# Performance work log

Measured on AMD Instinct MI355X. Metric: run time of the kernel, lower is better.

The kernel has to match this reference:

```python
import jax, jax.numpy as jnp
import numpy as np

D_MODEL = 2816
D_DENSE = 2112
N_EXPERTS = 128
G = 16
P = 8
D_FFN = 704
EPS = 1e-6
TOP_K = 8
H = 16
DH = 256
NKV = 8
MAX_CTX = 4096
WINDOW = 1024


def rmsnorm(x, w=None):
    h = x.astype(jnp.float32)
    h = h * jax.lax.rsqrt(jnp.mean(h * h, axis=-1, keepdims=True) + EPS)
    if w is not None:
        h = h * (1.0 + w.astype(jnp.float32))
    return h.astype(x.dtype)


def apply_rope(x, cos, sin):
    # x: (1,T,heads,D); cos/sin: (1,T,D)
    cos = cos[:, :, None, :]
    sin = sin[:, :, None, :]
    d = x.shape[-1]
    x1, x2 = x[..., : d // 2], x[..., d // 2 :]
    rot = jnp.concatenate([-x2, x1], axis=-1)
    return x * cos + rot * sin


def setup_inputs() -> dict:
    key = jax.random.key(0)
    ks = iter(jax.random.split(key, 40))
    def rn(shape, s=0.02):
        return jax.random.normal(next(ks), shape, jnp.float32) * s
    pos = MAX_CTX - 1
    half = DH // 2
    inv = 1.0 / (10000.0 ** (np.arange(half, dtype=np.float32) / half))
    ang = pos * inv
    cos = jnp.asarray(np.concatenate([np.cos(ang), np.cos(ang)]).astype(np.float32))[None, None, :]
    sin = jnp.asarray(np.concatenate([np.sin(ang), np.sin(ang)]).astype(np.float32))[None, None, :]
    idx = np.arange(MAX_CTX)
    allowed = (idx <= pos) & (idx > pos - WINDOW)
    attn_mask = jnp.asarray(np.where(allowed, 0.0, -1e9).astype(np.float32))[None, None, None, :]
    wm = np.zeros((1, 1, MAX_CTX, 1), np.float32)
    wm[0, 0, pos, 0] = 1.0
    return {
        "x": rn((1, 1, D_MODEL), 1.0),
        "cos": cos,
        "sin": sin,
        "k_cache": rn((1, NKV, MAX_CTX, DH), 0.02),
        "v_cache": rn((1, NKV, MAX_CTX, DH), 0.02),
        "attn_mask": attn_mask,
        "kv_write_mask": jnp.asarray(wm),
        "input_ln_w": rn((D_MODEL,), 0.1),
        "post_attn_ln_w": rn((D_MODEL,), 0.1),
        "pre_ffn_ln_w": rn((D_MODEL,), 0.1),
        "post_ffn_ln_1_w": rn((D_MODEL,), 0.1),
        "pre_ffn_ln_2_w": rn((D_MODEL,), 0.1),
        "post_ffn_ln_2_w": rn((D_MODEL,), 0.1),
        "post_ffn_ln_w": rn((D_MODEL,), 0.1),
        "Wq": rn((H * DH, D_MODEL)),
        "Wk": rn((NKV * DH, D_MODEL)),
        "Wv": rn((NKV * DH, D_MODEL)),
        "Wo": rn((D_MODEL, H * DH)),
        "q_norm_w": rn((DH,), 0.1),
        "k_norm_w": rn((DH,), 0.1),
        "dense_Wg": rn((D_DENSE, D_MODEL)),
        "dense_Wu": rn((D_DENSE, D_MODEL)),
        "dense_Wd": rn((D_MODEL, D_DENSE)),
        "router_Wp": rn((N_EXPERTS, D_MODEL)),
        "router_scale": jnp.ones((D_MODEL,), jnp.float32),
        "router_pes": jnp.ones((N_EXPERTS,), jnp.float32),
        "packs_Wg": rn((P, G * D_FFN, D_MODEL)),
        "packs_Wu": rn((P, G * D_FFN, D_MODEL)),
        "packs_Wd": rn((P, G * D_MODEL, D_FFN)),
        "layer_scalar": jnp.ones((1,), jnp.float32),
    }


def reference(x, cos, sin, k_cache, v_cache, attn_mask, kv_write_mask,
              input_ln_w, post_attn_ln_w, pre_ffn_ln_w, post_ffn_ln_1_w,
              pre_ffn_ln_2_w, post_ffn_ln_2_w, post_ffn_ln_w,
              Wq, Wk, Wv, Wo, q_norm_w, k_norm_w,
              dense_Wg, dense_Wu, dense_Wd,
              router_Wp, router_scale, router_pes,
              packs_Wg, packs_Wu, packs_Wd, layer_scalar):
    # ---- attention block ----
    residual = x
    h = rmsnorm(x, input_ln_w)
    q = (h @ Wq.T).reshape(1, 1, H, DH)
    k = (h @ Wk.T).reshape(1, 1, NKV, DH)
    v = (h @ Wv.T).reshape(1, 1, NKV, DH)
    q = apply_rope(rmsnorm(q, q_norm_w), cos, sin)
    k = apply_rope(rmsnorm(k, k_norm_w), cos, sin)
    v = rmsnorm(v)
    q = q.transpose(0, 2, 1, 3)            # (1,H,1,DH)
    k = k.transpose(0, 2, 1, 3)            # (1,NKV,1,DH)
    v = v.transpose(0, 2, 1, 3)
    k_new = k_cache + k * kv_write_mask    # one-hot write at current pos
    v_new = v_cache + v * kv_write_mask
    rep = H // NKV
    K = jnp.repeat(k_new, rep, axis=1)     # (1,H,CTX,DH)
    V = jnp.repeat(v_new, rep, axis=1)
    scores = jnp.einsum('bhqd,bhkd->bhqk', q, K) + attn_mask
    w = jax.nn.softmax(scores.astype(jnp.float32), axis=-1).astype(q.dtype)
    ctx = jnp.einsum('bhqk,bhkd->bhqd', w, V)
    ctx = ctx.transpose(0, 2, 1, 3).reshape(1, 1, H * DH)
    a = ctx @ Wo.T
    x1 = residual + rmsnorm(a, post_attn_ln_w)
    # ---- FFN block ----
    res2 = x1
    pre = rmsnorm(x1, pre_ffn_ln_w)
    dense = (jax.nn.gelu(pre @ dense_Wg.T, approximate=True) * (pre @ dense_Wu.T)) @ dense_Wd.T
    h1 = rmsnorm(dense, post_ffn_ln_1_w)
    # router (top-k over 128 experts, scatter to dense weights)
    hr = rmsnorm(res2) * router_scale * (D_MODEL ** -0.5)
    prob = jax.nn.softmax(jnp.einsum('btd,ed->bte', hr, router_Wp), axis=-1)
    topw, topi = jax.lax.top_k(prob, TOP_K)
    topw = topw / jnp.sum(topw, axis=-1, keepdims=True)
    topw = topw * router_pes[topi]
    onehot = (topi[..., None] == jnp.arange(N_EXPERTS)).astype(topw.dtype)
    rw = jnp.sum(topw[..., None] * onehot, axis=-2)          # (1,1,128)
    # packed experts: block-diagonal form of the GxG batched GEMM + diagonal gather
    pre2 = rmsnorm(res2, pre_ffn_ln_2_w)
    xv = pre2.reshape(D_MODEL)
    g = jax.nn.gelu(jnp.einsum('d,pfd->pf', xv, packs_Wg), approximate=True)
    u = jnp.einsum('d,pfd->pf', xv, packs_Wu)
    hh = (g * u).reshape(P, G, D_FFN)
    Wd3 = packs_Wd.reshape(P, G, D_MODEL, D_FFN)
    per_e = jnp.einsum('pgf,pgdf->pgd', hh, Wd3)             # per-expert outputs
    moe = jnp.einsum('pg,pgd->d', rw.reshape(P, G), per_e).reshape(1, 1, D_MODEL)
    h2 = rmsnorm(moe, post_ffn_ln_2_w)
    x_ffn = rmsnorm(h1 + h2, post_ffn_ln_w)
    out = (res2 + x_ffn) * layer_scalar
    return (out, k_new, v_new)
```

## Files before the change

### kernel.cpp

```cpp
#include <hip/hip_runtime.h>
#include <hip/hip_bf16.h>
#include <math.h>

#define D_MODEL 2816
#define DM4 704
#define D_DENSE 2112
#define N_EXPERTS 128
#define D_FFN 704
#define DF4 176
#define TOPK 8
#define H 16
#define DH 256
#define NKV 8
#define MAX_CTX 4096
#define EPS 1e-6f

__device__ __forceinline__ float wsum(float v){
  #pragma unroll
  for(int o=32;o>0;o>>=1) v += __shfl_down(v, o, 64);
  return v;
}
__device__ __forceinline__ float wmax(float v){
  #pragma unroll
  for(int o=32;o>0;o>>=1) v = fmaxf(v, __shfl_down(v, o, 64));
  return v;
}
__device__ __forceinline__ float wsum_all(float v){
  #pragma unroll
  for(int o=32;o>0;o>>=1) v += __shfl_xor(v, o, 64);
  return v;
}
__device__ __forceinline__ float wmax_all(float v){
  #pragma unroll
  for(int o=32;o>0;o>>=1) v = fmaxf(v, __shfl_xor(v, o, 64));
  return v;
}
__device__ __forceinline__ int wmin_all_i(int v){
  #pragma unroll
  for(int o=32;o>0;o>>=1) v = min(v, __shfl_xor(v, o, 64));
  return v;
}
__device__ __forceinline__ float block_sum(float v, float* sm){
  int lane = threadIdx.x & 63, w = threadIdx.x >> 6;
  int nw = blockDim.x >> 6;
  v = wsum(v);
  __syncthreads();
  if (lane == 0) sm[w] = v;
  __syncthreads();
  float t = 0.f;
  for (int i = 0; i < nw; i++) t += sm[i];
  return t;
}
__device__ __forceinline__ float gelu_tanh(float x){
  float x3 = x*x*x;
  return 0.5f*x*(1.f + tanhf(0.7978845608028654f*(x + 0.044715f*x3)));
}
__device__ __forceinline__ float dot4(float4 a, float4 b){
  return fmaf(a.x,b.x, fmaf(a.y,b.y, fmaf(a.z,b.z, a.w*b.w)));
}

__global__ __launch_bounds__(256) void k_qkv(const float* __restrict__ Wq,
    const float* __restrict__ Wk, const float* __restrict__ Wv,
    const float* __restrict__ x, const float* __restrict__ lw,
    float* __restrict__ out){
  __shared__ float sh[D_MODEL];
  __shared__ float sm[8];
  int t = threadIdx.x;
  float xv[11]; float ss = 0.f;
  #pragma unroll
  for (int i=0;i<11;i++){ xv[i] = x[t + 256*i]; ss += xv[i]*xv[i]; }
  ss = block_sum(ss, sm);
  float r = rsqrtf(ss/(float)D_MODEL + EPS);
  #pragma unroll
  for (int i=0;i<11;i++){ int idx=t+256*i; sh[idx] = xv[i]*r*(1.f+lw[idx]); }
  __syncthreads();

  int row = blockIdx.x*4 + (t>>6);
  int lane = t & 63;
  const float* W; int rr;
  if (row < 4096){ W=Wq; rr=row; }
  else if (row < 6144){ W=Wk; rr=row-4096; }
  else { W=Wv; rr=row-6144; }
  const float4* wr = (const float4*)(W + (size_t)rr*D_MODEL);
  const float4* hv = (const float4*)sh;
  float acc=0.f;
  for (int i=lane;i<DM4;i+=64) acc += dot4(wr[i], hv[i]);
  acc = wsum(acc);
  if (lane==0) out[row]=acc;
}

__global__ __launch_bounds__(256) void k_headnorm(const float* __restrict__ qkv,
    const float* __restrict__ qw, const float* __restrict__ kw,
    const float* __restrict__ cs, const float* __restrict__ sn,
    float* __restrict__ qf, float* __restrict__ kf, float* __restrict__ vf){
  __shared__ float sm[8];
  __shared__ float nb[DH];
  int b = blockIdx.x, t = threadIdx.x;
  const float* src; float* dst; const float* w = nullptr; bool rope=false;
  if (b < 16){ src=qkv + b*DH; dst=qf + b*DH; w=qw; rope=true; }
  else if (b < 24){ int hh=b-16; src=qkv+4096+hh*DH; dst=kf+hh*DH; w=kw; rope=true; }
  else { int hh=b-24; src=qkv+6144+hh*DH; dst=vf+hh*DH; }
  float v = src[t];
  float ss = block_sum(v*v, sm);
  float r = rsqrtf(ss/(float)DH + EPS);
  float nv = v*r*(w ? (1.f+w[t]) : 1.f);
  nb[t]=nv;
  __syncthreads();
  float o = nv;
  if (rope){
    float rot = (t < 128) ? -nb[t+128] : nb[t-128];
    o = nv*cs[t] + rot*sn[t];
  }
  dst[t]=o;
}

__global__ __launch_bounds__(256) void k_kvattn(const float* __restrict__ kc,
    const float* __restrict__ vc, const float* __restrict__ kf,
    const float* __restrict__ vf, const float* __restrict__ qf,
    const float* __restrict__ wm, const float* __restrict__ mask,
    float* __restrict__ ko, float* __restrict__ vo, float* __restrict__ part){
  int bid = blockIdx.x;
  if (bid < 4096){
    const size_t TOT = (size_t)NKV*MAX_CTX*(DH/4);
    const size_t stride = (size_t)4096*256;
    for (size_t i = (size_t)bid*256 + threadIdx.x; i < 2*TOT; i += stride){
      int isv = i >= TOT;
      size_t j = isv ? i - TOT : i;
      int pos  = (int)((j >> 6) & (MAX_CTX-1));
      int head = (int)(j >> 18);
      int d4   = (int)(j & 63);
      float m = wm[pos];
      float4 c = ((const float4*)(isv ? vc : kc))[j];
      float4 a = ((const float4*)((isv ? vf : kf) + head*DH))[d4];
      c.x = fmaf(a.x, m, c.x); c.y = fmaf(a.y, m, c.y);
      c.z = fmaf(a.z, m, c.z); c.w = fmaf(a.w, m, c.w);
      ((float4*)(isv ? vo : ko))[j] = c;
    }
    return;
  }
  __shared__ float sc[256];
  __shared__ float sw[256];
  __shared__ float sm[8];
  int abid = bid - 4096;
  int head = abid >> 4, chunk = abid & 15;
  int kvh = head >> 1;
  int lane = threadIdx.x & 63, wv = threadIdx.x >> 6;
  int t = threadIdx.x;
  int base = chunk*256;
  float mk_t = mask[base + t];
  float live = block_sum((mk_t > -1e8f) ? 1.f : 0.f, sm);
  float* p = part + (size_t)(head*16+chunk)*258;
  if (live == 0.f){
    if (t == 0){ p[0] = -3.0e38f; p[1] = 0.f; }
    return;
  }
  float4 q  = ((const float4*)(qf + head*DH))[lane];
  float4 kp = ((const float4*)(kf + kvh*DH))[lane];
  float vp  = vf[kvh*DH + t];
  const float* K = kc + (size_t)kvh*MAX_CTX*DH;
  const float* V = vc + (size_t)kvh*MAX_CTX*DH;
  for (int i=0;i<64;i++){
    int pp = wv*64 + i;
    int pos = base + pp;
    float mk = mask[pos];
    float s = -3.0e38f;
    if (mk > -1e8f){
      float m = wm[pos];
      float4 kv = ((const float4*)(K + (size_t)pos*DH))[lane];
      kv.x = fmaf(kp.x, m, kv.x); kv.y = fmaf(kp.y, m, kv.y);
      kv.z = fmaf(kp.z, m, kv.z); kv.w = fmaf(kp.w, m, kv.w);
      float d = wsum(dot4(q, kv));
      s = d + mk;
    }
    if (lane==0) sc[pp] = s;
  }
  __syncthreads();
  float sv = sc[t];
  float mx = wmax(sv);
  __syncthreads();
  if (lane==0) sm[wv]=mx;
  __syncthreads();
  mx = fmaxf(fmaxf(sm[0],sm[1]),fmaxf(sm[2],sm[3]));
  float w = (sv > -1e30f) ? __expf(sv - mx) : 0.f;
  sw[t] = w;
  float ssum = block_sum(w, sm);
  float acc = 0.f;
  for (int i=0;i<256;i++){
    float wi = sw[i];
    if (wi != 0.f){
      float v = fmaf(vp, wm[base+i], V[(size_t)(base+i)*DH + t]);
      acc = fmaf(wi, v, acc);
    }
  }
  if (t==0){ p[0]=mx; p[1]=ssum; }
  p[2+t]=acc;
}

__global__ __launch_bounds__(256) void k_attn_comb(const float* __restrict__ part,
    float* __restrict__ ctx){
  int head = blockIdx.x, t = threadIdx.x;
  float M = -3.0e38f;
  for (int c=0;c<16;c++) M = fmaxf(M, part[(size_t)(head*16+c)*258]);
  float tot = 0.f, acc = 0.f;
  for (int c=0;c<16;c++){
    const float* p = part + (size_t)(head*16+c)*258;
    float mc=p[0], scv=p[1];
    if (scv > 0.f){
      float f = __expf(mc - M);
      tot = fmaf(scv, f, tot);
      acc = fmaf(f, p[2+t], acc);
    }
  }
  ctx[head*DH + t] = acc / tot;
}

__global__ __launch_bounds__(256) void k_gemv(const float* __restrict__ W,
    const float* __restrict__ x, float* __restrict__ y, int rows, int k4){
  int row = blockIdx.x*4 + (threadIdx.x>>6);
  int lane = threadIdx.x & 63;
  if (row >= rows) return;
  const float4* wr = (const float4*)W + (size_t)row*k4;
  const float4* xv = (const float4*)x;
  float acc = 0.f;
  for (int i=lane;i<k4;i+=64) acc += dot4(wr[i], xv[i]);
  acc = wsum(acc);
  if (lane==0) y[row]=acc;
}

__global__ __launch_bounds__(256) void k_postattn(const float* __restrict__ a,
    const float* __restrict__ x, const float* __restrict__ wpost,
    const float* __restrict__ wpre, const float* __restrict__ rscale,
    const float* __restrict__ wpre2,
    float* __restrict__ x1, float* __restrict__ pre,
    float* __restrict__ hr, float* __restrict__ pre2){
  __shared__ float sm[8];
  int t = threadIdx.x;
  float av[11]; float ss=0.f;
  #pragma unroll
  for (int i=0;i<11;i++){ av[i]=a[t+256*i]; ss += av[i]*av[i]; }
  ss = block_sum(ss, sm);
  float ra = rsqrtf(ss/(float)D_MODEL + EPS);
  float xv[11]; float ss2=0.f;
  #pragma unroll
  for (int i=0;i<11;i++){
    int idx=t+256*i;
    xv[i] = x[idx] + av[i]*ra*(1.f+wpost[idx]);
    ss2 += xv[i]*xv[i];
  }
  ss2 = block_sum(ss2, sm);
  float r1 = rsqrtf(ss2/(float)D_MODEL + EPS);
  const float invsq = rsqrtf((float)D_MODEL);
  #pragma unroll
  for (int i=0;i<11;i++){
    int idx=t+256*i;
    float n = xv[i]*r1;
    x1[idx]=xv[i];
    pre[idx]=n*(1.f+wpre[idx]);
    hr[idx]=n*rscale[idx]*invsq;
    pre2[idx]=n*(1.f+wpre2[idx]);
  }
}

__global__ __launch_bounds__(256) void k_dense_gu_router(const float* __restrict__ Wg,
    const float* __restrict__ Wu, const float* __restrict__ pre,
    const float* __restrict__ Wp, const float* __restrict__ hr,
    float* __restrict__ act, float* __restrict__ lg){
  int lane = threadIdx.x & 63;
  int wv = threadIdx.x >> 6;
  if (blockIdx.x < 528){
    int row = blockIdx.x*4 + wv;
    const float4* g4 = (const float4*)(Wg + (size_t)row*D_MODEL);
    const float4* u4 = (const float4*)(Wu + (size_t)row*D_MODEL);
    const float4* xv = (const float4*)pre;
    float ag=0.f, au=0.f;
    for (int i=lane;i<DM4;i+=64){
      float4 b = xv[i];
      ag += dot4(g4[i], b);
      au += dot4(u4[i], b);
    }
    ag = wsum(ag); au = wsum(au);
    if (lane==0) act[row] = gelu_tanh(ag)*au;
  } else {
    int row = (blockIdx.x-528)*4 + wv;
    const float4* wr = (const float4*)(Wp + (size_t)row*D_MODEL);
    const float4* xv = (const float4*)hr;
    float acc = 0.f;
    for (int i=lane;i<DM4;i+=64) acc += dot4(wr[i], xv[i]);
    acc = wsum(acc);
    if (lane==0) lg[row]=acc;
  }
}

__global__ __launch_bounds__(64) void k_topk(const float* __restrict__ lg,
    const float* __restrict__ pes, float* __restrict__ selw, int* __restrict__ seli){
  int lane = threadIdx.x;
  float l0 = lg[lane], l1 = lg[lane+64];
  float m = wmax_all(fmaxf(l0,l1));
  float e0 = __expf(l0-m), e1 = __expf(l1-m);
  float s = wsum_all(e0+e1);
  float p0 = e0/s, p1 = e1/s;
  float vals[8]; int idxs[8]; float tw=0.f;
  #pragma unroll
  for (int ts=0;ts<8;ts++){
    float mx = wmax_all(fmaxf(p0,p1));
    int cand = 0x7fffffff;
    if (p0 == mx) cand = lane;
    else if (p1 == mx) cand = lane + 64;
    int imin = wmin_all_i(cand);
    if (imin == lane) p0 = -1.f;
    else if (imin == lane+64) p1 = -1.f;
    vals[ts]=mx; idxs[ts]=imin; tw += mx;
  }
  if (lane == 0){
    #pragma unroll
    for (int ts=0;ts<8;ts++){
      selw[ts] = vals[ts]/tw*pes[idxs[ts]];
      seli[ts] = idxs[ts];
    }
  }
}

__global__ __launch_bounds__(256) void k_ddown_moegu(const float* __restrict__ Wd,
    const float* __restrict__ act, float* __restrict__ dense,
    const float* __restrict__ pWg, const float* __restrict__ pWu,
    const float* __restrict__ pre2, const int* __restrict__ seli,
    float* __restrict__ hh){
  int lane = threadIdx.x & 63;
  int wv = threadIdx.x >> 6;
  if (blockIdx.x < 704){
    int row = blockIdx.x*4 + wv;
    const float4* wr = (const float4*)(Wd + (size_t)row*D_DENSE);
    const float4* xv = (const float4*)act;
    float acc = 0.f;
    for (int i=lane;i<528;i+=64) acc += dot4(wr[i], xv[i]);
    acc = wsum(acc);
    if (lane==0) dense[row]=acc;
  } else {
    int gidx = (blockIdx.x-704)*4 + wv;
    int sl = gidx / D_FFN;
    int f = gidx - sl*D_FFN;
    int e = seli[sl];
    int p = e >> 4, g = e & 15;
    size_t ro = ((size_t)p*(16*D_FFN) + (size_t)g*D_FFN + f)*D_MODEL;
    const float4* g4 = (const float4*)(pWg + ro);
    const float4* u4 = (const float4*)(pWu + ro);
    const float4* xv = (const float4*)pre2;
    float ag=0.f, au=0.f;
    for (int i=lane;i<DM4;i+=64){
      float4 b=xv[i];
      ag += dot4(g4[i], b);
      au += dot4(u4[i], b);
    }
    ag = wsum(ag); au = wsum(au);
    if (lane==0) hh[sl*D_FFN + f] = gelu_tanh(ag)*au;
  }
}

__global__ __launch_bounds__(256) void k_moe_down(const float* __restrict__ Wd,
    const float* __restrict__ hh, const int* __restrict__ seli,
    float* __restrict__ pere){
  int gidx = blockIdx.x*4 + (threadIdx.x>>6);
  int lane = threadIdx.x & 63;
  int sl = gidx / D_MODEL;
  int d = gidx - sl*D_MODEL;
  int e = seli[sl];
  int p = e >> 4, g = e & 15;
  const float4* wr = (const float4*)(Wd + ((size_t)p*(16*D_MODEL) + (size_t)g*D_MODEL + d)*D_FFN);
  const float4* xv = (const float4*)(hh + sl*D_FFN);
  float acc=0.f;
  for (int i=lane;i<DF4;i+=64) acc += dot4(wr[i], xv[i]);
  acc = wsum(acc);
  if (lane==0) pere[sl*D_MODEL + d] = acc;
}

__global__ __launch_bounds__(256) void k_final(const float* __restrict__ pere,
    const float* __restrict__ selw, const float* __restrict__ dense,
    const float* __restrict__ x1, const float* __restrict__ w2,
    const float* __restrict__ w1, const float* __restrict__ wf,
    const float* __restrict__ lsc, float* __restrict__ out){
  __shared__ float sm[8];
  int t = threadIdx.x;
  float mo[11], dn[11]; float ssm_=0.f, ssd=0.f;
  #pragma unroll
  for (int i=0;i<11;i++){
    int idx=t+256*i;
    float mv=0.f;
    #pragma unroll
    for (int s=0;s<TOPK;s++) mv = fmaf(selw[s], pere[s*D_MODEL+idx], mv);
    mo[i]=mv; ssm_ += mv*mv;
    dn[i]=dense[idx]; ssd += dn[i]*dn[i];
  }
  ssm_ = block_sum(ssm_, sm);
  ssd = block_sum(ssd, sm);
  float rm = rsqrtf(ssm_/(float)D_MODEL + EPS);
  float rd = rsqrtf(ssd/(float)D_MODEL + EPS);
  float tv[11]; float sst=0.f;
  #pragma unroll
  for (int i=0;i<11;i++){
    int idx=t+256*i;
    float h2 = mo[i]*rm*(1.f+w2[idx]);
    float h1 = dn[i]*rd*(1.f+w1[idx]);
    tv[i]=h1+h2; sst += tv[i]*tv[i];
  }
  sst = block_sum(sst, sm);
  float rt = rsqrtf(sst/(float)D_MODEL + EPS);
  float l = lsc[0];
  #pragma unroll
  for (int i=0;i<11;i++){
    int idx=t+256*i;
    out[idx] = (x1[idx] + tv[i]*rt*(1.f+wf[idx]))*l;
  }
}

extern "C" void kernel_launch(void* const* d_in, const int* in_sizes, int n_in,
                              void* d_out, int out_size, void* d_ws, size_t ws_size,
                              hipStream_t stream){
  const float* x        = (const float*)d_in[0];
  const float* cs       = (const float*)d_in[1];
  const float* sn       = (const float*)d_in[2];
  const float* kc       = (const float*)d_in[3];
  const float* vc       = (const float*)d_in[4];
  const float* mask     = (const float*)d_in[5];
  const float* wm       = (const float*)d_in[6];
  const float* in_ln    = (const float*)d_in[7];
  const float* post_attn= (const float*)d_in[8];
  const float* pre_ffn  = (const float*)d_in[9];
  const float* post_ffn1= (const float*)d_in[10];
  const float* pre_ffn2 = (const float*)d_in[11];
  const float* post_ffn2= (const float*)d_in[12];
  const float* post_ffn = (const float*)d_in[13];
  const float* Wq       = (const float*)d_in[14];
  const float* Wk       = (const float*)d_in[15];
  const float* Wv       = (const float*)d_in[16];
  const float* Wo       = (const float*)d_in[17];
  const float* qnw      = (const float*)d_in[18];
  const float* knw      = (const float*)d_in[19];
  const float* dWg      = (const float*)d_in[20];
  const float* dWu      = (const float*)d_in[21];
  const float* dWd      = (const float*)d_in[22];
  const float* rWp      = (const float*)d_in[23];
  const float* rscale   = (const float*)d_in[24];
  const float* rpes     = (const float*)d_in[25];
  const float* pWg      = (const float*)d_in[26];
  const float* pWu      = (const float*)d_in[27];
  const float* pWd      = (const float*)d_in[28];
  const float* lsc      = (const float*)d_in[29];

  float* out = (float*)d_out;
  float* ko  = out + D_MODEL;
  float* vo  = ko + (size_t)NKV*MAX_CTX*DH;

  float* ws   = (float*)d_ws;
  float* qkv  = ws + 0;
  float* qf   = ws + 8192;
  float* kf   = ws + 12288;
  float* vf   = ws + 14336;
  float* ctx  = ws + 16384;
  float* a    = ws + 20480;
  float* x1   = ws + 23296;
  float* pre  = ws + 26112;
  float* hr   = ws + 28928;
  float* pre2 = ws + 31744;
  float* act  = ws + 34560;
  float* dense= ws + 36672;
  float* lg   = ws + 39488;
  float* selw = ws + 39616;
  int*   seli = (int*)(ws + 39624);
  float* hh   = ws + 39632;
  float* pere = ws + 45264;
  float* part = ws + 67792;

  k_qkv            <<<2048, 256, 0, stream>>>(Wq, Wk, Wv, x, in_ln, qkv);
  k_headnorm       <<<32,   256, 0, stream>>>(qkv, qnw, knw, cs, sn, qf, kf, vf);
  k_kvattn         <<<4352, 256, 0, stream>>>(kc, vc, kf, vf, qf, wm, mask, ko, vo, part);
  k_attn_comb      <<<16,   256, 0, stream>>>(part, ctx);
  k_gemv           <<<704,  256, 0, stream>>>(Wo, ctx, a, D_MODEL, 1024);
  k_postattn       <<<1,    256, 0, stream>>>(a, x, post_attn, pre_ffn, rscale, pre_ffn2,
                                              x1, pre, hr, pre2);
  k_dense_gu_router<<<560,  256, 0, stream>>>(dWg, dWu, pre, rWp, hr, act, lg);
  k_topk           <<<1,     64, 0, stream>>>(lg, rpes, selw, seli);
  k_ddown_moegu    <<<2112, 256, 0, stream>>>(dWd, act, dense, pWg, pWu, pre2, seli, hh);
  k_moe_down       <<<5632, 256, 0, stream>>>(pWd, hh, seli, pere);
  k_final          <<<1,    256, 0, stream>>>(pere, selw, dense, x1,
                                              post_ffn2, post_ffn1, post_ffn, lsc, out);
}
```

Measured before the change: 254.3 us.

## Fuse small kernels via last-block atomic counters, cutting launches from eleven to six

Merges headnorm into the attention/KV-copy kernel, with each block recomputing its own q/k/v normalization and RoPE. The attention combine, post-attention norm, top-k and final norm are moved into the tail of the preceding kernels using a threadfence plus atomic counter, so the last block to finish does the reduction. Counters are zeroed in the first kernel. This removes several tiny single-block launches and their gaps, at the cost of redundant head-norm work per block and a serialized tail block in each fused kernel.

New measurement: 781.9 us. +207.5%, slower.

```diff
diff --git a/kernel.cpp b/kernel.cpp
--- a/kernel.cpp
+++ b/kernel.cpp
@@ -62,10 +62,11 @@
 __global__ __launch_bounds__(256) void k_qkv(const float* __restrict__ Wq,
     const float* __restrict__ Wk, const float* __restrict__ Wv,
     const float* __restrict__ x, const float* __restrict__ lw,
-    float* __restrict__ out){
+    float* __restrict__ out, int* __restrict__ cnt){
   __shared__ float sh[D_MODEL];
   __shared__ float sm[8];
   int t = threadIdx.x;
+  if (blockIdx.x == 0 && t < 32) cnt[t] = 0;
   float xv[11]; float ss = 0.f;
   #pragma unroll
   for (int i=0;i<11;i++){ xv[i] = x[t + 256*i]; ss += xv[i]*xv[i]; }
@@ -89,184 +90,223 @@
   if (lane==0) out[row]=acc;
 }
 
-__global__ __launch_bounds__(256) void k_headnorm(const float* __restrict__ qkv,
+__global__ __launch_bounds__(256) void k_attn_copy(
+    const float* __restrict__ kc, const float* __restrict__ vc,
+    const float* __restrict__ qkv,
     const float* __restrict__ qw, const float* __restrict__ kw,
     const float* __restrict__ cs, const float* __restrict__ sn,
-    float* __restrict__ qf, float* __restrict__ kf, float* __restrict__ vf){
+    const float* __restrict__ wm, const float* __restrict__ mask,
+    float* __restrict__ ko, float* __restrict__ vo,
+    float* __restrict__ part, float* __restrict__ ctx, int* __restrict__ cnt){
   __shared__ float sm[8];
-  __shared__ float nb[DH];
-  int b = blockIdx.x, t = threadIdx.x;
-  const float* src; float* dst; const float* w = nullptr; bool rope=false;
-  if (b < 16){ src=qkv + b*DH; dst=qf + b*DH; w=qw; rope=true; }
-  else if (b < 24){ int hh=b-16; src=qkv+4096+hh*DH; dst=kf+hh*DH; w=kw; rope=true; }
-  else { int hh=b-24; src=qkv+6144+hh*DH; dst=vf+hh*DH; }
-  float v = src[t];
-  float ss = block_sum(v*v, sm);
-  float r = rsqrtf(ss/(float)DH + EPS);
-  float nv = v*r*(w ? (1.f+w[t]) : 1.f);
-  nb[t]=nv;
-  __syncthreads();
-  float o = nv;
-  if (rope){
-    float rot = (t < 128) ? -nb[t+128] : nb[t-128];
-    o = nv*cs[t] + rot*sn[t];
-  }
-  dst[t]=o;
-}
-
-__global__ __launch_bounds__(256) void k_kvattn(const float* __restrict__ kc,
-    const float* __restrict__ vc, const float* __restrict__ kf,
-    const float* __restrict__ vf, const float* __restrict__ qf,
-    const float* __restrict__ wm, const float* __restrict__ mask,
-    float* __restrict__ ko, float* __restrict__ vo, float* __restrict__ part){
-  int bid = blockIdx.x;
-  if (bid < 4096){
-    const size_t TOT = (size_t)NKV*MAX_CTX*(DH/4);
-    const size_t stride = (size_t)4096*256;
-    for (size_t i = (size_t)bid*256 + threadIdx.x; i < 2*TOT; i += stride){
-      int isv = i >= TOT;
-      size_t j = isv ? i - TOT : i;
-      int pos  = (int)((j >> 6) & (MAX_CTX-1));
-      int head = (int)(j >> 18);
-      int d4   = (int)(j & 63);
+  int t = threadIdx.x;
+
+  if (blockIdx.x >= 256){
+    __shared__ float nrm[DH];
+    int b = blockIdx.x - 256;
+    int tensor = b >> 11;
+    int head = (b >> 8) & 7;
+    int blk = b & 255;
+    const float* src = qkv + (tensor ? 6144 : 4096) + head*DH;
+    float v = src[t];
+    float ssq = block_sum(v*v, sm);
+    float r = rsqrtf(ssq/(float)DH + EPS);
+    float base_ = v*r*(tensor==0 ? (1.f+kw[t]) : 1.f);
+    nrm[t] = base_;
+    __syncthreads();
+    float nv = base_;
+    if (tensor == 0){
+      float rot = (t<128) ? -nrm[t+128] : nrm[t-128];
+      nv = base_*cs[t] + rot*sn[t];
+    }
+    __syncthreads();
+    nrm[t] = nv;
+    __syncthreads();
+    const float4* cache = (const float4*)(tensor ? vc : kc);
+    float4* outp = (float4*)(tensor ? vo : ko);
+    const float4* a4 = (const float4*)nrm;
+    size_t hb = (size_t)head * (MAX_CTX*(DH/4));
+    int lbase = blk*1024;
+    #pragma unroll
+    for (int q=0;q<4;q++){
+      int jl = lbase + q*256 + t;
+      int pos = jl >> 6;
+      int d4 = jl & 63;
       float m = wm[pos];
-      float4 c = ((const float4*)(isv ? vc : kc))[j];
-      float4 a = ((const float4*)((isv ? vf : kf) + head*DH))[d4];
-      c.x = fmaf(a.x, m, c.x); c.y = fmaf(a.y, m, c.y);
-      c.z = fmaf(a.z, m, c.z); c.w = fmaf(a.w, m, c.w);
-      ((float4*)(isv ? vo : ko))[j] = c;
+      float4 c = cache[hb + jl];
+      float4 a = a4[d4];
+      c.x = fmaf(a.x,m,c.x); c.y = fmaf(a.y,m,c.y);
+      c.z = fmaf(a.z,m,c.z); c.w = fmaf(a.w,m,c.w);
+      outp[hb + jl] = c;
     }
     return;
   }
-  __shared__ float sc[256];
-  __shared__ float sw[256];
-  __shared__ float sm[8];
-  int abid = bid - 4096;
-  int head = abid >> 4, chunk = abid & 15;
+
+  __shared__ float qrow[DH], krow[DH], vrow[DH], sc[256], sw[256];
+  int head = blockIdx.x >> 4, chunk = blockIdx.x & 15;
   int kvh = head >> 1;
-  int lane = threadIdx.x & 63, wv = threadIdx.x >> 6;
-  int t = threadIdx.x;
+  int lane = t & 63, wv = t >> 6;
+
+  {
+    float v = qkv[head*DH + t];
+    float ssq = block_sum(v*v, sm);
+    float r = rsqrtf(ssq/(float)DH + EPS);
+    float b_ = v*r*(1.f+qw[t]);
+    qrow[t]=b_;
+    __syncthreads();
+    float rot = (t<128) ? -qrow[t+128] : qrow[t-128];
+    float nv = b_*cs[t] + rot*sn[t];
+    __syncthreads();
+    qrow[t]=nv;
+  }
+  {
+    float v = qkv[4096 + kvh*DH + t];
+    float ssq = block_sum(v*v, sm);
+    float r = rsqrtf(ssq/(float)DH + EPS);
+    float b_ = v*r*(1.f+kw[t]);
+    krow[t]=b_;
+    __syncthreads();
+    float rot = (t<128) ? -krow[t+128] : krow[t-128];
+    float nv = b_*cs[t] + rot*sn[t];
+    __syncthreads();
+    krow[t]=nv;
+  }
+  {
+    float v = qkv[6144 + kvh*DH + t];
+    float ssq = block_sum(v*v, sm);
+    vrow[t] = v*rsqrtf(ssq/(float)DH + EPS);
+  }
+  __syncthreads();
+
   int base = chunk*256;
   float mk_t = mask[base + t];
   float live = block_sum((mk_t > -1e8f) ? 1.f : 0.f, sm);
   float* p = part + (size_t)(head*16+chunk)*258;
-  if (live == 0.f){
+  if (live != 0.f){
+    float4 q  = ((const float4*)qrow)[lane];
+    float4 kp = ((const float4*)krow)[lane];
+    float vp  = vrow[t];
+    const float* K = kc + (size_t)kvh*MAX_CTX*DH;
+    const float* V = vc + (size_t)kvh*MAX_CTX*DH;
+    for (int i=0;i<64;i++){
+      int pp = wv*64 + i;
+      int pos = base + pp;
+      float mk = mask[pos];
+      float s = -3.0e38f;
+      if (mk > -1e8f){
+        float m = wm[pos];
+        float4 kv = ((const float4*)(K + (size_t)pos*DH))[lane];
+        kv.x = fmaf(kp.x, m, kv.x); kv.y = fmaf(kp.y, m, kv.y);
+        kv.z = fmaf(kp.z, m, kv.z); kv.w = fmaf(kp.w, m, kv.w);
+        float d = wsum(dot4(q, kv));
+        s = d + mk;
+      }
+      if (lane==0) sc[pp] = s;
+    }
+    __syncthreads();
+    float sv = sc[t];
+    float mx = wmax(sv);
+    __syncthreads();
+    if (lane==0) sm[wv]=mx;
+    __syncthreads();
+    mx = fmaxf(fmaxf(sm[0],sm[1]),fmaxf(sm[2],sm[3]));
+    float w = (sv > -1e30f) ? __expf(sv - mx) : 0.f;
+    sw[t] = w;
+    float ssum = block_sum(w, sm);
+    float acc = 0.f;
+    for (int i=0;i<256;i++){
+      float wi = sw[i];
+      if (wi != 0.f){
+        float v = fmaf(vp, wm[base+i], V[(size_t)(base+i)*DH + t]);
+        acc = fmaf(wi, v, acc);
+      }
+    }
+    if (t==0){ p[0]=mx; p[1]=ssum; }
+    p[2+t]=acc;
+  } else {
     if (t == 0){ p[0] = -3.0e38f; p[1] = 0.f; }
-    return;
-  }
-  float4 q  = ((const float4*)(qf + head*DH))[lane];
-  float4 kp = ((const float4*)(kf + kvh*DH))[lane];
-  float vp  = vf[kvh*DH + t];
-  const float* K = kc + (size_t)kvh*MAX_CTX*DH;
-  const float* V = vc + (size_t)kvh*MAX_CTX*DH;
-  for (int i=0;i<64;i++){
-    int pp = wv*64 + i;
-    int pos = base + pp;
-    float mk = mask[pos];
-    float s = -3.0e38f;
-    if (mk > -1e8f){
-      float m = wm[pos];
-      float4 kv = ((const float4*)(K + (size_t)pos*DH))[lane];
-      kv.x = fmaf(kp.x, m, kv.x); kv.y = fmaf(kp.y, m, kv.y);
-      kv.z = fmaf(kp.z, m, kv.z); kv.w = fmaf(kp.w, m, kv.w);
-      float d = wsum(dot4(q, kv));
-      s = d + mk;
-    }
-    if (lane==0) sc[pp] = s;
-  }
-  __syncthreads();
-  float sv = sc[t];
-  float mx = wmax(sv);
-  __syncthreads();
-  if (lane==0) sm[wv]=mx;
-  __syncthreads();
-  mx = fmaxf(fmaxf(sm[0],sm[1]),fmaxf(sm[2],sm[3]));
-  float w = (sv > -1e30f) ? __expf(sv - mx) : 0.f;
-  sw[t] = w;
-  float ssum = block_sum(w, sm);
+  }
+
+  __threadfence();
+  __syncthreads();
+  __shared__ int lastf;
+  if (t==0) lastf = (atomicAdd(&cnt[head],1) == 15);
+  __syncthreads();
+  if (lastf){
+    __threadfence();
+    float M = -3.0e38f;
+    for (int c=0;c<16;c++) M = fmaxf(M, part[(size_t)(head*16+c)*258]);
+    float tot = 0.f, acc = 0.f;
+    for (int c=0;c<16;c++){
+      const float* pc = part + (size_t)(head*16+c)*258;
+      float mc=pc[0], scv=pc[1];
+      if (scv > 0.f){
+        float f = __expf(mc - M);
+        tot = fmaf(scv, f, tot);
+        acc = fmaf(f, pc[2+t], acc);
+      }
+    }
+    ctx[head*DH + t] = acc / tot;
+  }
+}
+
+__global__ __launch_bounds__(256) void k_wo_post(const float* __restrict__ Wo,
+    const float* __restrict__ ctxv, const float* __restrict__ x,
+    const float* __restrict__ wpost, const float* __restrict__ wpre,
+    const float* __restrict__ rscale, const float* __restrict__ wpre2,
+    float* __restrict__ a, float* __restrict__ x1, float* __restrict__ pre,
+    float* __restrict__ hr, float* __restrict__ pre2, int* __restrict__ cnt){
+  __shared__ float sm[8];
+  int t = threadIdx.x, lane = t & 63, wv = t >> 6;
+  int row = blockIdx.x*4 + wv;
+  const float4* wr = (const float4*)(Wo + (size_t)row*4096);
+  const float4* xv = (const float4*)ctxv;
   float acc = 0.f;
-  for (int i=0;i<256;i++){
-    float wi = sw[i];
-    if (wi != 0.f){
-      float v = fmaf(vp, wm[base+i], V[(size_t)(base+i)*DH + t]);
-      acc = fmaf(wi, v, acc);
-    }
-  }
-  if (t==0){ p[0]=mx; p[1]=ssum; }
-  p[2+t]=acc;
-}
-
-__global__ __launch_bounds__(256) void k_attn_comb(const float* __restrict__ part,
-    float* __restrict__ ctx){
-  int head = blockIdx.x, t = threadIdx.x;
-  float M = -3.0e38f;
-  for (int c=0;c<16;c++) M = fmaxf(M, part[(size_t)(head*16+c)*258]);
-  float tot = 0.f, acc = 0.f;
-  for (int c=0;c<16;c++){
-    const float* p = part + (size_t)(head*16+c)*258;
-    float mc=p[0], scv=p[1];
-    if (scv > 0.f){
-      float f = __expf(mc - M);
-      tot = fmaf(scv, f, tot);
-      acc = fmaf(f, p[2+t], acc);
-    }
-  }
-  ctx[head*DH + t] = acc / tot;
-}
-
-__global__ __launch_bounds__(256) void k_gemv(const float* __restrict__ W,
-    const float* __restrict__ x, float* __restrict__ y, int rows, int k4){
-  int row = blockIdx.x*4 + (threadIdx.x>>6);
-  int lane = threadIdx.x & 63;
-  if (row >= rows) return;
-  const float4* wr = (const float4*)W + (size_t)row*k4;
-  const float4* xv = (const float4*)x;
-  float acc = 0.f;
-  for (int i=lane;i<k4;i+=64) acc += dot4(wr[i], xv[i]);
+  for (int i=lane;i<1024;i+=64) acc += dot4(wr[i], xv[i]);
   acc = wsum(acc);
-  if (lane==0) y[row]=acc;
-}
-
-__global__ __launch_bounds__(256) void k_postattn(const float* __restrict__ a,
-    const float* __restrict__ x, const float* __restrict__ wpost,
-    const float* __restrict__ wpre, const float* __restrict__ rscale,
-    const float* __restrict__ wpre2,
-    float* __restrict__ x1, float* __restrict__ pre,
-    float* __restrict__ hr, float* __restrict__ pre2){
-  __shared__ float sm[8];
-  int t = threadIdx.x;
-  float av[11]; float ss=0.f;
-  #pragma unroll
-  for (int i=0;i<11;i++){ av[i]=a[t+256*i]; ss += av[i]*av[i]; }
-  ss = block_sum(ss, sm);
-  float ra = rsqrtf(ss/(float)D_MODEL + EPS);
-  float xv[11]; float ss2=0.f;
-  #pragma unroll
-  for (int i=0;i<11;i++){
-    int idx=t+256*i;
-    xv[i] = x[idx] + av[i]*ra*(1.f+wpost[idx]);
-    ss2 += xv[i]*xv[i];
-  }
-  ss2 = block_sum(ss2, sm);
-  float r1 = rsqrtf(ss2/(float)D_MODEL + EPS);
-  const float invsq = rsqrtf((float)D_MODEL);
-  #pragma unroll
-  for (int i=0;i<11;i++){
-    int idx=t+256*i;
-    float n = xv[i]*r1;
-    x1[idx]=xv[i];
-    pre[idx]=n*(1.f+wpre[idx]);
-    hr[idx]=n*rscale[idx]*invsq;
-    pre2[idx]=n*(1.f+wpre2[idx]);
-  }
-}
-
-__global__ __launch_bounds__(256) void k_dense_gu_router(const float* __restrict__ Wg,
+  if (lane==0) a[row]=acc;
+
+  __threadfence();
+  __syncthreads();
+  __shared__ int lastf;
+  if (t==0) lastf = (atomicAdd(&cnt[16],1) == 703);
+  __syncthreads();
+  if (lastf){
+    __threadfence();
+    float av[11]; float ss=0.f;
+    #pragma unroll
+    for (int i=0;i<11;i++){ av[i]=a[t+256*i]; ss += av[i]*av[i]; }
+    ss = block_sum(ss, sm);
+    float ra = rsqrtf(ss/(float)D_MODEL + EPS);
+    float xvv[11]; float ss2=0.f;
+    #pragma unroll
+    for (int i=0;i<11;i++){
+      int idx=t+256*i;
+      xvv[i] = x[idx] + av[i]*ra*(1.f+wpost[idx]);
+      ss2 += xvv[i]*xvv[i];
+    }
+    ss2 = block_sum(ss2, sm);
+    float r1 = rsqrtf(ss2/(float)D_MODEL + EPS);
+    const float invsq = rsqrtf((float)D_MODEL);
+    #pragma unroll
+    for (int i=0;i<11;i++){
+      int idx=t+256*i;
+      float n = xvv[i]*r1;
+      x1[idx]=xvv[i];
+      pre[idx]=n*(1.f+wpre[idx]);
+      hr[idx]=n*rscale[idx]*invsq;
+      pre2[idx]=n*(1.f+wpre2[idx]);
+    }
+  }
+}
+
+__global__ __launch_bounds__(256) void k_dense_router(const float* __restrict__ Wg,
     const float* __restrict__ Wu, const float* __restrict__ pre,
     const float* __restrict__ Wp, const float* __restrict__ hr,
-    float* __restrict__ act, float* __restrict__ lg){
-  int lane = threadIdx.x & 63;
-  int wv = threadIdx.x >> 6;
+    const float* __restrict__ pes,
+    float* __restrict__ act, float* __restrict__ lg,
+    float* __restrict__ selw, int* __restrict__ seli, int* __restrict__ cnt){
+  int t = threadIdx.x, lane = t & 63, wv = t >> 6;
   if (blockIdx.x < 528){
     int row = blockIdx.x*4 + wv;
     const float4* g4 = (const float4*)(Wg + (size_t)row*D_MODEL);
@@ -280,42 +320,49 @@
     }
     ag = wsum(ag); au = wsum(au);
     if (lane==0) act[row] = gelu_tanh(ag)*au;
-  } else {
-    int row = (blockIdx.x-528)*4 + wv;
-    const float4* wr = (const float4*)(Wp + (size_t)row*D_MODEL);
-    const float4* xv = (const float4*)hr;
-    float acc = 0.f;
-    for (int i=lane;i<DM4;i+=64) acc += dot4(wr[i], xv[i]);
-    acc = wsum(acc);
-    if (lane==0) lg[row]=acc;
-  }
-}
-
-__global__ __launch_bounds__(64) void k_topk(const float* __restrict__ lg,
-    const float* __restrict__ pes, float* __restrict__ selw, int* __restrict__ seli){
-  int lane = threadIdx.x;
-  float l0 = lg[lane], l1 = lg[lane+64];
-  float m = wmax_all(fmaxf(l0,l1));
-  float e0 = __expf(l0-m), e1 = __expf(l1-m);
-  float s = wsum_all(e0+e1);
-  float p0 = e0/s, p1 = e1/s;
-  float vals[8]; int idxs[8]; float tw=0.f;
-  #pragma unroll
-  for (int ts=0;ts<8;ts++){
-    float mx = wmax_all(fmaxf(p0,p1));
-    int cand = 0x7fffffff;
-    if (p0 == mx) cand = lane;
-    else if (p1 == mx) cand = lane + 64;
-    int imin = wmin_all_i(cand);
-    if (imin == lane) p0 = -1.f;
-    else if (imin == lane+64) p1 = -1.f;
-    vals[ts]=mx; idxs[ts]=imin; tw += mx;
-  }
-  if (lane == 0){
-    #pragma unroll
-    for (int ts=0;ts<8;ts++){
-      selw[ts] = vals[ts]/tw*pes[idxs[ts]];
-      seli[ts] = idxs[ts];
+    return;
+  }
+  int row = (blockIdx.x-528)*4 + wv;
+  const float4* wr = (const float4*)(Wp + (size_t)row*D_MODEL);
+  const float4* xv = (const float4*)hr;
+  float acc = 0.f;
+  for (int i=lane;i<DM4;i+=64) acc += dot4(wr[i], xv[i]);
+  acc = wsum(acc);
+  if (lane==0) lg[row]=acc;
+
+  __threadfence();
+  __syncthreads();
+  __shared__ int lastf;
+  if (t==0) lastf = (atomicAdd(&cnt[17],1) == 31);
+  __syncthreads();
+  if (lastf){
+    __threadfence();
+    if (t < 64){
+      int ln = t;
+      float l0 = lg[ln], l1 = lg[ln+64];
+      float m = wmax_all(fmaxf(l0,l1));
+      float e0 = __expf(l0-m), e1 = __expf(l1-m);
+      float s = wsum_all(e0+e1);
+      float p0 = e0/s, p1 = e1/s;
+      float vals[8]; int idxs[8]; float tw=0.f;
+      #pragma unroll
+      for (int ts=0;ts<8;ts++){
+        float mx = wmax_all(fmaxf(p0,p1));
+        int cand = 0x7fffffff;
+        if (p0 == mx) cand = ln;
+        else if (p1 == mx) cand = ln + 64;
+        int imin = wmin_all_i(cand);
+        if (imin == ln) p0 = -1.f;
+        else if (imin == ln+64) p1 = -1.f;
+        vals[ts]=mx; idxs[ts]=imin; tw += mx;
+      }
+      if (ln == 0){
+        #pragma unroll
+        for (int ts=0;ts<8;ts++){
+          selw[ts] = vals[ts]/tw*pes[idxs[ts]];
+          seli[ts] = idxs[ts];
+        }
+      }
     }
   }
 }
@@ -356,11 +403,17 @@
   }
 }
 
-__global__ __launch_bounds__(256) void k_moe_down(const float* __restrict__ Wd,
+__global__ __launch_bounds__(256) void k_moedown_final(const float* __restrict__ Wd,
     const float* __restrict__ hh, const int* __restrict__ seli,
-    float* __restrict__ pere){
-  int gidx = blockIdx.x*4 + (threadIdx.x>>6);
-  int lane = threadIdx.x & 63;
+    float* __restrict__ pere,
+    const float* __restrict__ selw, const float* __restrict__ dense,
+    const float* __restrict__ x1, const float* __restrict__ w2,
+    const float* __restrict__ w1, const float* __restrict__ wf,
+    const float* __restrict__ lsc, float* __restrict__ out, int* __restrict__ cnt){
+  __shared__ float sm[8];
+  int t = threadIdx.x;
+  int gidx = blockIdx.x*4 + (t>>6);
+  int lane = t & 63;
   int sl = gidx / D_MODEL;
   int d = gidx - sl*D_MODEL;
   int e = seli[sl];
@@ -371,44 +424,44 @@
   for (int i=lane;i<DF4;i+=64) acc += dot4(wr[i], xv[i]);
   acc = wsum(acc);
   if (lane==0) pere[sl*D_MODEL + d] = acc;
-}
-
-__global__ __launch_bounds__(256) void k_final(const float* __restrict__ pere,
-    const float* __restrict__ selw, const float* __restrict__ dense,
-    const float* __restrict__ x1, const float* __restrict__ w2,
-    const float* __restrict__ w1, const float* __restrict__ wf,
-    const float* __restrict__ lsc, float* __restrict__ out){
-  __shared__ float sm[8];
-  int t = threadIdx.x;
-  float mo[11], dn[11]; float ssm_=0.f, ssd=0.f;
-  #pragma unroll
-  for (int i=0;i<11;i++){
-    int idx=t+256*i;
-    float mv=0.f;
-    #pragma unroll
-    for (int s=0;s<TOPK;s++) mv = fmaf(selw[s], pere[s*D_MODEL+idx], mv);
-    mo[i]=mv; ssm_ += mv*mv;
-    dn[i]=dense[idx]; ssd += dn[i]*dn[i];
-  }
-  ssm_ = block_sum(ssm_, sm);
-  ssd = block_sum(ssd, sm);
-  float rm = rsqrtf(ssm_/(float)D_MODEL + EPS);
-  float rd = rsqrtf(ssd/(float)D_MODEL + EPS);
-  float tv[11]; float sst=0.f;
-  #pragma unroll
-  for (int i=0;i<11;i++){
-    int idx=t+256*i;
-    float h2 = mo[i]*rm*(1.f+w2[idx]);
-    float h1 = dn[i]*rd*(1.f+w1[idx]);
-    tv[i]=h1+h2; sst += tv[i]*tv[i];
-  }
-  sst = block_sum(sst, sm);
-  float rt = rsqrtf(sst/(float)D_MODEL + EPS);
-  float l = lsc[0];
-  #pragma unroll
-  for (int i=0;i<11;i++){
-    int idx=t+256*i;
-    out[idx] = (x1[idx] + tv[i]*rt*(1.f+wf[idx]))*l;
+
+  __threadfence();
+  __syncthreads();
+  __shared__ int lastf;
+  if (t==0) lastf = (atomicAdd(&cnt[18],1) == 5631);
+  __syncthreads();
+  if (lastf){
+    __threadfence();
+    float mo[11], dn[11]; float ssm_=0.f, ssd=0.f;
+    #pragma unroll
+    for (int i=0;i<11;i++){
+      int idx=t+256*i;
+      float mv=0.f;
+      #pragma unroll
+      for (int s=0;s<TOPK;s++) mv = fmaf(selw[s], pere[s*D_MODEL+idx], mv);
+      mo[i]=mv; ssm_ += mv*mv;
+      dn[i]=dense[idx]; ssd += dn[i]*dn[i];
+    }
+    ssm_ = block_sum(ssm_, sm);
+    ssd = block_sum(ssd, sm);
+    float rm = rsqrtf(ssm_/(float)D_MODEL + EPS);
+    float rd = rsqrtf(ssd/(float)D_MODEL + EPS);
+    float tv[11]; float sst=0.f;
+    #pragma unroll
+    for (int i=0;i<11;i++){
+      int idx=t+256*i;
+      float h2 = mo[i]*rm*(1.f+w2[idx]);
+      float h1 = dn[i]*rd*(1.f+w1[idx]);
+      tv[i]=h1+h2; sst += tv[i]*tv[i];
+    }
+    sst = block_sum(sst, sm);
+    float rt = rsqrtf(sst/(float)D_MODEL + EPS);
+    float l = lsc[0];
+    #pragma unroll
+    for (int i=0;i<11;i++){
+      int idx=t+256*i;
+      out[idx] = (x1[idx] + tv[i]*rt*(1.f+wf[idx]))*l;
+    }
   }
 }
 
@@ -452,9 +505,6 @@
 
   float* ws   = (float*)d_ws;
   float* qkv  = ws + 0;
-  float* qf   = ws + 8192;
-  float* kf   = ws + 12288;
-  float* vf   = ws + 14336;
   float* ctx  = ws + 16384;
   float* a    = ws + 20480;
   float* x1   = ws + 23296;
@@ -469,18 +519,16 @@
   float* hh   = ws + 39632;
   float* pere = ws + 45264;
   float* part = ws + 67792;
-
-  k_qkv            <<<2048, 256, 0, stream>>>(Wq, Wk, Wv, x, in_ln, qkv);
-  k_headnorm       <<<32,   256, 0, stream>>>(qkv, qnw, knw, cs, sn, qf, kf, vf);
-  k_kvattn         <<<4352, 256, 0, stream>>>(kc, vc, kf, vf, qf, wm, mask, ko, vo, part);
-  k_attn_comb      <<<16,   256, 0, stream>>>(part, ctx);
-  k_gemv           <<<704,  256, 0, stream>>>(Wo, ctx, a, D_MODEL, 1024);
-  k_postattn       <<<1,    256, 0, stream>>>(a, x, post_attn, pre_ffn, rscale, pre_ffn2,
-                                              x1, pre, hr, pre2);
-  k_dense_gu_router<<<560,  256, 0, stream>>>(dWg, dWu, pre, rWp, hr, act, lg);
-  k_topk           <<<1,     64, 0, stream>>>(lg, rpes, selw, seli);
-  k_ddown_moegu    <<<2112, 256, 0, stream>>>(dWd, act, dense, pWg, pWu, pre2, seli, hh);
-  k_moe_down       <<<5632, 256, 0, stream>>>(pWd, hh, seli, pere);
-  k_final          <<<1,    256, 0, stream>>>(pere, selw, dense, x1,
-                                              post_ffn2, post_ffn1, post_ffn, lsc, out);
-}
+  int*   cnt  = (int*)(ws + 133840);
+
+  k_qkv           <<<2048, 256, 0, stream>>>(Wq, Wk, Wv, x, in_ln, qkv, cnt);
+  k_attn_copy     <<<4352, 256, 0, stream>>>(kc, vc, qkv, qnw, knw, cs, sn, wm, mask,
+                                             ko, vo, part, ctx, cnt);
+  k_wo_post       <<<704,  256, 0, stream>>>(Wo, ctx, x, post_attn, pre_ffn, rscale,
+                                             pre_ffn2, a, x1, pre, hr, pre2, cnt);
+  k_dense_router  <<<560,  256, 0, stream>>>(dWg, dWu, pre, rWp, hr, rpes,
+                                             act, lg, selw, seli, cnt);
+  k_ddown_moegu   <<<2112, 256, 0, stream>>>(dWd, act, dense, pWg, pWu, pre2, seli, hh);
+  k_moedown_final <<<5632, 256, 0, stream>>>(pWd, hh, seli, pere, selw, dense, x1,
+                                             post_ffn2, post_ffn1, post_ffn, lsc, out, cnt);
+}
```
